# Kernel tuning notes

Measured on AMD Instinct MI355X. Metric: run time of the kernel, lower is better.

Reference implementation:

```python
import jax, jax.numpy as jnp
import numpy as np

NUM_STAGES = 3
EPS = 1e-6


def _l2norm(x, axis):
    return x / (EPS + jnp.linalg.norm(x, axis=axis, keepdims=True))


def _l1norm(x, axis):
    return x / (EPS + jnp.sum(x, axis=axis, keepdims=True))


def setup_inputs() -> dict:
    key = jax.random.key(0)
    k1, k2 = jax.random.split(key)
    B, C, H, W, K = 16, 512, 64, 64, 64
    feats = jax.random.normal(k1, (B, C, H, W), dtype=jnp.float32)
    # bases buffer: N(0, sqrt(2/K)) then l2-normalized along channel dim (done in reference)
    bases = jax.random.normal(k2, (1, C, K), dtype=jnp.float32) * np.sqrt(2.0 / K)
    return {"feats": feats, "bases": bases}


def reference(feats, bases):
    B, C, H, W = feats.shape
    f = feats.reshape(B, C, H * W)              # [B, C, N]
    b = _l2norm(bases, axis=1)                  # match buffer init normalization
    b = jnp.broadcast_to(b, (B, C, b.shape[2])) # [B, C, K]
    attention = None
    for _ in range(NUM_STAGES):
        attention = jnp.einsum('bcn,bck->bnk', f, b)        # [B, N, K]
        attention = jax.nn.softmax(attention, axis=2)
        attention_normed = _l1norm(attention, axis=1)
        b = jnp.einsum('bcn,bnk->bck', f, attention_normed)  # [B, C, K]
        b = _l2norm(b, axis=1)
    # EM loop runs under torch.no_grad in the original
    b = jax.lax.stop_gradient(b)
    attention = jax.lax.stop_gradient(attention)
    feats_recon = jnp.einsum('bck,bnk->bcn', b, attention)   # [B, C, N]
    return feats_recon.reshape(B, C, H, W)
```

## Files before the change

### kernel.cpp

```cpp
#include <hip/hip_runtime.h>
#include <stdint.h>

#define B_ 16
#define C_ 512
#define N_ 4096
#define K_ 64
#define NUM_STAGES 3

typedef __bf16 bf16x8 __attribute__((ext_vector_type(8)));
typedef float f32x4 __attribute__((ext_vector_type(4)));

__device__ __forceinline__ uint16_t f2bf(float x) {
  union { float f; uint32_t u; } v; v.f = x;
  uint32_t r = (v.u + 0x7FFFu + ((v.u >> 16) & 1u)) >> 16;
  return (uint16_t)r;
}

__device__ __forceinline__ void async16(const uint16_t* g, uint16_t* l) {
  __builtin_amdgcn_global_load_lds(
      (const __attribute__((address_space(1))) unsigned int*)g,
      (__attribute__((address_space(3))) unsigned int*)l, 16, 0, 0);
}

__global__ __launch_bounds__(256) void k_prep(const float* __restrict__ feats,
                                              uint16_t* __restrict__ f16,
                                              uint16_t* __restrict__ fT16) {
  __shared__ uint16_t tile[64][65];
  int b = blockIdx.z, c0 = blockIdx.y * 64, n0 = blockIdx.x * 64;
  int t = threadIdx.x;
  const float* src = feats + ((size_t)b * C_ + c0) * N_ + n0;
  uint16_t* dst = f16 + ((size_t)b * C_ + c0) * N_ + n0;
  int cl = t >> 4;
  int nl = (t & 15) * 4;
#pragma unroll
  for (int i = 0; i < 4; ++i) {
    int c = cl + 16 * i;
    float4 v = *(const float4*)(src + (size_t)c * N_ + nl);
    ushort4 x;
    x.x = f2bf(v.x); x.y = f2bf(v.y); x.z = f2bf(v.z); x.w = f2bf(v.w);
    *(ushort4*)(dst + (size_t)c * N_ + nl) = x;
    tile[c][nl + 0] = x.x; tile[c][nl + 1] = x.y;
    tile[c][nl + 2] = x.z; tile[c][nl + 3] = x.w;
  }
  __syncthreads();
  uint16_t* dstT = fT16 + ((size_t)b * N_ + n0) * C_ + c0;
#pragma unroll
  for (int i = 0; i < 4; ++i) {
    int n = cl + 16 * i;
    int c = nl;
    ushort4 y;
    y.x = tile[c + 0][n]; y.y = tile[c + 1][n];
    y.z = tile[c + 2][n]; y.w = tile[c + 3][n];
    *(ushort4*)(dstT + (size_t)n * C_ + c) = y;
  }
}

__global__ __launch_bounds__(256) void k_init_basis(const float* __restrict__ bases,
                                                    uint16_t* __restrict__ basis,
                                                    uint16_t* __restrict__ basisT) {
  int b = blockIdx.x;
  int t = threadIdx.x;
  __shared__ float red[256];
  __shared__ float inv[64];
  int k = t & 63;
  float s = 0.f;
  for (int c = (t >> 6); c < C_; c += 4) {
    float v = bases[c * K_ + k];
    s += v * v;
  }
  red[t] = s;
  __syncthreads();
  if (t < 64) {
    float tot = red[t] + red[t + 64] + red[t + 128] + red[t + 192];
    inv[t] = 1.f / (1e-6f + sqrtf(tot));
  }
  __syncthreads();
  uint16_t* ob = basis + (size_t)b * C_ * K_;
  for (int i = 0; i < (C_ * K_) / 256; ++i) {
    int idx = t + 256 * i;
    int kk = idx & 63;
    ob[idx] = f2bf(bases[idx] * inv[kk]);
  }
  uint16_t* obT = basisT + (size_t)b * K_ * C_;
  for (int i = 0; i < (C_ * K_) / 256; ++i) {
    int idx = t + 256 * i;
    int kk = idx >> 9;
    int cc = idx & 511;
    obT[idx] = f2bf(bases[cc * K_ + kk] * inv[kk]);
  }
}

__global__ __launch_bounds__(256) void k_gemm1(const uint16_t* __restrict__ fT,
                                               const uint16_t* __restrict__ basisT,
                                               uint16_t* __restrict__ attn,
                                               uint16_t* __restrict__ attnT,
                                               int write_attn) {
  __shared__ __attribute__((aligned(16))) uint16_t ldsA[64 * 64];
  __shared__ __attribute__((aligned(16))) uint16_t ldsB[64 * 64];
  int b = blockIdx.y;
  int n0 = blockIdx.x * 64;
  int t = threadIdx.x;
  int w = t >> 6, lane = t & 63, l15 = lane & 15, quad = lane >> 4;
  const uint16_t* A = fT + ((size_t)b * N_ + n0) * C_;
  const uint16_t* Bm = basisT + (size_t)b * K_ * C_;
  f32x4 acc[4] = {};
  for (int cs = 0; cs < C_; cs += 64) {
    __syncthreads();
#pragma unroll
    for (int r = 0; r < 2; ++r) {
      int e = r * 256 + t;
      int row = e >> 3, ch = e & 7;
      int sch = (ch + row) & 7;
      async16(A + (size_t)row * C_ + cs + sch * 8, ldsA + (r * 256 + (t & 192)) * 8);
    }
#pragma unroll
    for (int r = 0; r < 2; ++r) {
      int e = r * 256 + t;
      int row = e >> 3, ch = e & 7;
      int sch = (ch + row) & 7;
      async16(Bm + (size_t)row * C_ + cs + sch * 8, ldsB + (r * 256 + (t & 192)) * 8);
    }
    __syncthreads();
#pragma unroll
    for (int s = 0; s < 2; ++s) {
      int cc = s * 4 + quad;
      int ra = 16 * w + l15;
      bf16x8 af = *(const bf16x8*)(ldsA + (ra * 8 + ((cc - ra) & 7)) * 8);
#pragma unroll
      for (int t4 = 0; t4 < 4; ++t4) {
        int rb = 16 * t4 + l15;
        bf16x8 bv = *(const bf16x8*)(ldsB + (rb * 8 + ((cc - rb) & 7)) * 8);
        acc[t4] = __builtin_amdgcn_mfma_f32_16x16x32_bf16(af, bv, acc[t4], 0, 0, 0);
      }
    }
  }
  float p[4][4];
#pragma unroll
  for (int r = 0; r < 4; ++r) {
    float m = fmaxf(fmaxf(acc[0][r], acc[1][r]), fmaxf(acc[2][r], acc[3][r]));
    m = fmaxf(m, __shfl_xor(m, 1));
    m = fmaxf(m, __shfl_xor(m, 2));
    m = fmaxf(m, __shfl_xor(m, 4));
    m = fmaxf(m, __shfl_xor(m, 8));
    float s = 0.f;
#pragma unroll
    for (int t4 = 0; t4 < 4; ++t4) { p[t4][r] = __expf(acc[t4][r] - m); s += p[t4][r]; }
    s += __shfl_xor(s, 1); s += __shfl_xor(s, 2);
    s += __shfl_xor(s, 4); s += __shfl_xor(s, 8);
    float inv = 1.f / s;
#pragma unroll
    for (int t4 = 0; t4 < 4; ++t4) p[t4][r] *= inv;
  }
  if (write_attn) {
    uint16_t* oa = attn + ((size_t)b * N_ + n0 + 16 * w + quad * 4) * K_;
#pragma unroll
    for (int r = 0; r < 4; ++r) {
#pragma unroll
      for (int t4 = 0; t4 < 4; ++t4) oa[(size_t)r * K_ + 16 * t4 + l15] = f2bf(p[t4][r]);
    }
  }
#pragma unroll
  for (int t4 = 0; t4 < 4; ++t4) {
    ushort4 y;
    y.x = f2bf(p[t4][0]); y.y = f2bf(p[t4][1]);
    y.z = f2bf(p[t4][2]); y.w = f2bf(p[t4][3]);
    *(ushort4*)(attnT + ((size_t)b * K_ + 16 * t4 + l15) * N_ + n0 + 16 * w + quad * 4) = y;
  }
}

__global__ __launch_bounds__(256) void k_gemm2(const uint16_t* __restrict__ f16,
                                               const uint16_t* __restrict__ attnT,
                                               float* __restrict__ brawT) {
  __shared__ __attribute__((aligned(16))) uint16_t ldsA[32 * 64];
  __shared__ __attribute__((aligned(16))) uint16_t ldsB[64 * 64];
  int b = blockIdx.z;
  int c0 = blockIdx.x * 32;
  int slice = blockIdx.y;
  int ns0 = slice * 1024;
  int t = threadIdx.x, w = t >> 6, lane = t & 63, l15 = lane & 15, quad = lane >> 4;
  int h = w >> 1, kh = w & 1;
  const uint16_t* A = f16 + ((size_t)b * C_ + c0) * N_;
  const uint16_t* Bm = attnT + (size_t)b * K_ * N_;
  f32x4 acc[2] = {};
  for (int ns = ns0; ns < ns0 + 1024; ns += 64) {
    __syncthreads();
    {
      int row = t >> 3, ch = t & 7;
      int sch = (ch + row) & 7;
      async16(A + (size_t)row * N_ + ns + sch * 8, ldsA + (t & 192) * 8);
    }
#pragma unroll
    for (int r = 0; r < 2; ++r) {
      int e = r * 256 + t;
      int row = e >> 3, ch = e & 7;
      int sch = (ch + row) & 7;
      async16(Bm + (size_t)row * N_ + ns + sch * 8, ldsB + (r * 256 + (t & 192)) * 8);
    }
    __syncthreads();
#pragma unroll
    for (int s = 0; s < 2; ++s) {
      int cc = s * 4 + quad;
      int ra = 16 * h + l15;
      bf16x8 af = *(const bf16x8*)(ldsA + (ra * 8 + ((cc - ra) & 7)) * 8);
#pragma unroll
      for (int t2 = 0; t2 < 2; ++t2) {
        int rb = 32 * kh + 16 * t2 + l15;
        bf16x8 bv = *(const bf16x8*)(ldsB + (rb * 8 + ((cc - rb) & 7)) * 8);
        acc[t2] = __builtin_amdgcn_mfma_f32_16x16x32_bf16(af, bv, acc[t2], 0, 0, 0);
      }
    }
  }
  float* out = brawT + ((size_t)slice * B_ + b) * K_ * C_;
#pragma unroll
  for (int t2 = 0; t2 < 2; ++t2) {
    int k = 32 * kh + 16 * t2 + l15;
    float4 v = make_float4(acc[t2][0], acc[t2][1], acc[t2][2], acc[t2][3]);
    *(float4*)(out + (size_t)k * C_ + c0 + 16 * h + quad * 4) = v;
  }
}

__global__ __launch_bounds__(256) void k_l2fused(const float* __restrict__ brawT,
                                                 uint16_t* __restrict__ basisT,
                                                 uint16_t* __restrict__ basis) {
  __shared__ float red[4][128];
  __shared__ float invs[4];
  int b = blockIdx.x, kg = blockIdx.y;
  int t = threadIdx.x;
  int c4 = (t & 127) * 4;
  int khalf = t >> 7;
  float4 bs[2];
  float pr[2];
#pragma unroll
  for (int i = 0; i < 2; ++i) {
    int k = kg * 4 + khalf * 2 + i;
    float4 a = make_float4(0.f, 0.f, 0.f, 0.f);
#pragma unroll
    for (int s = 0; s < 4; ++s) {
      const float* rp = brawT + (((size_t)s * B_ + b) * K_ + k) * C_ + c4;
      float4 v = *(const float4*)rp;
      a.x += v.x; a.y += v.y; a.z += v.z; a.w += v.w;
    }
    bs[i] = a;
    pr[i] = a.x * a.x + a.y * a.y + a.z * a.z + a.w * a.w;
  }
  red[khalf * 2 + 0][t & 127] = pr[0];
  red[khalf * 2 + 1][t & 127] = pr[1];
  __syncthreads();
  if (t < 4) {
    float s = 0.f;
#pragma unroll
    for (int j = 0; j < 128; ++j) s += red[t][j];
    invs[t] = 1.f / (1e-6f + sqrtf(s));
  }
  __syncthreads();
#pragma unroll
  for (int i = 0; i < 2; ++i) {
    int kk = khalf * 2 + i;
    int k = kg * 4 + kk;
    float inv = invs[kk];
    ushort4 y;
    y.x = f2bf(bs[i].x * inv); y.y = f2bf(bs[i].y * inv);
    y.z = f2bf(bs[i].z * inv); y.w = f2bf(bs[i].w * inv);
    *(ushort4*)(basisT + ((size_t)b * K_ + k) * C_ + c4) = y;
    uint16_t* ob = basis + (size_t)b * C_ * K_ + k;
    ob[(size_t)(c4 + 0) * K_] = y.x;
    ob[(size_t)(c4 + 1) * K_] = y.y;
    ob[(size_t)(c4 + 2) * K_] = y.z;
    ob[(size_t)(c4 + 3) * K_] = y.w;
  }
}

__global__ __launch_bounds__(256) void k_recon(const uint16_t* __restrict__ attn,
                                               const uint16_t* __restrict__ basis,
                                               float* __restrict__ out) {
  __shared__ __attribute__((aligned(16))) char smem[64 * 68 * 4];
  uint16_t* ldsA = (uint16_t*)smem;
  uint16_t* ldsB = (uint16_t*)(smem + 8192);
  float* ldsT = (float*)smem;
  int b = blockIdx.z, c0 = blockIdx.y * 64, n0 = blockIdx.x * 64;
  int t = threadIdx.x, w = t >> 6, lane = t & 63, l15 = lane & 15, quad = lane >> 4;
  const uint16_t* A = attn + ((size_t)b * N_ + n0) * K_;
  const uint16_t* Bm = basis + ((size_t)b * C_ + c0) * K_;
#pragma unroll
  for (int r = 0; r < 2; ++r) {
    int e = r * 256 + t;
    int row = e >> 3, ch = e & 7, sch = (ch + row) & 7;
    async16(A + (size_t)row * K_ + sch * 8, ldsA + (r * 256 + (t & 192)) * 8);
  }
#pragma unroll
  for (int r = 0; r < 2; ++r) {
    int e = r * 256 + t;
    int row = e >> 3, ch = e & 7, sch = (ch + row) & 7;
    async16(Bm + (size_t)row * K_ + sch * 8, ldsB + (r * 256 + (t & 192)) * 8);
  }
  f32x4 acc[4] = {};
  __syncthreads();
#pragma unroll
  for (int s = 0; s < 2; ++s) {
    int cc = s * 4 + quad;
    int ra = 16 * w + l15;
    bf16x8 af = *(const bf16x8*)(ldsA + (ra * 8 + ((cc - ra) & 7)) * 8);
#pragma unroll
    for (int t4 = 0; t4 < 4; ++t4) {
      int rb = 16 * t4 + l15;
      bf16x8 bv = *(const bf16x8*)(ldsB + (rb * 8 + ((cc - rb) & 7)) * 8);
      acc[t4] = __builtin_amdgcn_mfma_f32_16x16x32_bf16(af, bv, acc[t4], 0, 0, 0);
    }
  }
  __syncthreads();
#pragma unroll
  for (int t4 = 0; t4 < 4; ++t4) {
    float4 v = make_float4(acc[t4][0], acc[t4][1], acc[t4][2], acc[t4][3]);
    *(float4*)(ldsT + (size_t)(16 * t4 + l15) * 68 + 16 * w + quad * 4) = v;
  }
  __syncthreads();
  float* op = out + ((size_t)b * C_ + c0) * N_ + n0;
#pragma unroll
  for (int j = 0; j < 16; ++j) {
    int c = 4 * j + w;
    op[(size_t)c * N_ + lane] = ldsT[(size_t)c * 68 + lane];
  }
}

extern "C" void kernel_launch(void* const* d_in, const int* in_sizes, int n_in,
                              void* d_out, int out_size, void* d_ws, size_t ws_size,
                              hipStream_t stream) {
  const float* feats = (const float*)d_in[0];
  const float* bases = (const float*)d_in[1];
  float* out = (float*)d_out;
  char* ws = (char*)d_ws;
  uint16_t* f16 = (uint16_t*)(ws);
  uint16_t* fT16 = (uint16_t*)(ws + 67108864);
  uint16_t* attn = (uint16_t*)(ws + 134217728);
  uint16_t* attnT = (uint16_t*)(ws + 142606336);
  uint16_t* basis = (uint16_t*)(ws + 150994944);
  uint16_t* basisT = (uint16_t*)(ws + 152043520);
  float* brawT = (float*)(ws + 153092096);

  k_prep<<<dim3(64, 8, 16), 256, 0, stream>>>(feats, f16, fT16);
  k_init_basis<<<16, 256, 0, stream>>>(bases, basis, basisT);
  for (int st = 0; st < NUM_STAGES; ++st) {
    k_gemm1<<<dim3(64, 16), 256, 0, stream>>>(fT16, basisT, attn, attnT,
                                              st == NUM_STAGES - 1 ? 1 : 0);
    k_gemm2<<<dim3(16, 4, 16), 256, 0, stream>>>(f16, attnT, brawT);
    k_l2fused<<<dim3(16, 16), 256, 0, stream>>>(brawT, basisT, basis);
  }
  k_recon<<<dim3(64, 8, 16), 256, 0, stream>>>(attn, basis, out);
}
```

Measured before the change: 447.6 us.

## Widen prep transpose tiles, vectorize recon stores, shuffle-reduce l2 norms

The prep kernel now handles 128x128 tiles with 16-byte loads and stores. It packs bf16 pairs into 32-bit words in an XOR-swizzled LDS tile, so the transposed write of fT16 uses full 16-byte stores instead of 8-byte ones. The recon epilogue writes float4 per thread instead of scalar floats. The l2 norm reduction replaces a serial 128-element loop on four threads with wave shuffles. These changes target memory-transaction efficiency and a serialized reduction, at the cost of fewer, larger prep blocks and more complex swizzle indexing.

```diff
diff --git a/kernel.cpp b/kernel.cpp
--- a/kernel.cpp
+++ b/kernel.cpp
@@ -25,33 +25,51 @@
 __global__ __launch_bounds__(256) void k_prep(const float* __restrict__ feats,
                                               uint16_t* __restrict__ f16,
                                               uint16_t* __restrict__ fT16) {
-  __shared__ uint16_t tile[64][65];
-  int b = blockIdx.z, c0 = blockIdx.y * 64, n0 = blockIdx.x * 64;
+  __shared__ uint32_t tile[128][64];
+  int b = blockIdx.z, c0 = blockIdx.y * 128, n0 = blockIdx.x * 128;
   int t = threadIdx.x;
+  int rl = t >> 4;
+  int g = t & 15;
   const float* src = feats + ((size_t)b * C_ + c0) * N_ + n0;
   uint16_t* dst = f16 + ((size_t)b * C_ + c0) * N_ + n0;
-  int cl = t >> 4;
-  int nl = (t & 15) * 4;
-#pragma unroll
-  for (int i = 0; i < 4; ++i) {
-    int c = cl + 16 * i;
-    float4 v = *(const float4*)(src + (size_t)c * N_ + nl);
-    ushort4 x;
-    x.x = f2bf(v.x); x.y = f2bf(v.y); x.z = f2bf(v.z); x.w = f2bf(v.w);
-    *(ushort4*)(dst + (size_t)c * N_ + nl) = x;
-    tile[c][nl + 0] = x.x; tile[c][nl + 1] = x.y;
-    tile[c][nl + 2] = x.z; tile[c][nl + 3] = x.w;
+#pragma unroll
+  for (int i = 0; i < 8; ++i) {
+    int c = rl + 16 * i;
+    int n8 = g * 8;
+    float4 v0 = *(const float4*)(src + (size_t)c * N_ + n8);
+    float4 v1 = *(const float4*)(src + (size_t)c * N_ + n8 + 4);
+    uint32_t q0 = (uint32_t)f2bf(v0.x) | ((uint32_t)f2bf(v0.y) << 16);
+    uint32_t q1 = (uint32_t)f2bf(v0.z) | ((uint32_t)f2bf(v0.w) << 16);
+    uint32_t q2 = (uint32_t)f2bf(v1.x) | ((uint32_t)f2bf(v1.y) << 16);
+    uint32_t q3 = (uint32_t)f2bf(v1.z) | ((uint32_t)f2bf(v1.w) << 16);
+    *(uint4*)(dst + (size_t)c * N_ + n8) = make_uint4(q0, q1, q2, q3);
+    int h = 2 * ((c >> 3) & 15);
+    int base = (4 * g) ^ (h & 28);
+    int p = h & 3;
+    uint32_t w[4];
+    w[0 ^ p] = q0; w[1 ^ p] = q1; w[2 ^ p] = q2; w[3 ^ p] = q3;
+    *(uint4*)&tile[c][base] = make_uint4(w[0], w[1], w[2], w[3]);
   }
   __syncthreads();
   uint16_t* dstT = fT16 + ((size_t)b * N_ + n0) * C_ + c0;
 #pragma unroll
-  for (int i = 0; i < 4; ++i) {
-    int n = cl + 16 * i;
-    int c = nl;
-    ushort4 y;
-    y.x = tile[c + 0][n]; y.y = tile[c + 1][n];
-    y.z = tile[c + 2][n]; y.w = tile[c + 3][n];
-    *(ushort4*)(dstT + (size_t)n * C_ + c) = y;
+  for (int i = 0; i < 8; ++i) {
+    int n = rl + 16 * i;
+    int s = n >> 1, half = (n & 1) * 16;
+    int c8 = g * 8;
+    uint16_t e[8];
+#pragma unroll
+    for (int j = 0; j < 8; ++j) {
+      int c = c8 + j;
+      int h = 2 * ((c >> 3) & 15);
+      uint32_t u = tile[c][s ^ h];
+      e[j] = (uint16_t)(u >> half);
+    }
+    uint32_t q0 = (uint32_t)e[0] | ((uint32_t)e[1] << 16);
+    uint32_t q1 = (uint32_t)e[2] | ((uint32_t)e[3] << 16);
+    uint32_t q2 = (uint32_t)e[4] | ((uint32_t)e[5] << 16);
+    uint32_t q3 = (uint32_t)e[6] | ((uint32_t)e[7] << 16);
+    *(uint4*)(dstT + (size_t)n * C_ + c8) = make_uint4(q0, q1, q2, q3);
   }
 }
 
@@ -225,7 +243,7 @@
   __shared__ float red[4][128];
   __shared__ float invs[4];
   int b = blockIdx.x, kg = blockIdx.y;
-  int t = threadIdx.x;
+  int t = threadIdx.x, lane = t & 63;
   int c4 = (t & 127) * 4;
   int khalf = t >> 7;
   float4 bs[2];
@@ -246,11 +264,12 @@
   red[khalf * 2 + 0][t & 127] = pr[0];
   red[khalf * 2 + 1][t & 127] = pr[1];
   __syncthreads();
-  if (t < 4) {
-    float s = 0.f;
-#pragma unroll
-    for (int j = 0; j < 128; ++j) s += red[t][j];
-    invs[t] = 1.f / (1e-6f + sqrtf(s));
+  {
+    int g = t >> 6;
+    float s = red[g][lane] + red[g][lane + 64];
+    s += __shfl_xor(s, 1); s += __shfl_xor(s, 2); s += __shfl_xor(s, 4);
+    s += __shfl_xor(s, 8); s += __shfl_xor(s, 16); s += __shfl_xor(s, 32);
+    if (lane == 0) invs[g] = 1.f / (1e-6f + sqrtf(s));
   }
   __syncthreads();
 #pragma unroll
@@ -315,10 +334,11 @@
   }
   __syncthreads();
   float* op = out + ((size_t)b * C_ + c0) * N_ + n0;
-#pragma unroll
-  for (int j = 0; j < 16; ++j) {
-    int c = 4 * j + w;
-    op[(size_t)c * N_ + lane] = ldsT[(size_t)c * 68 + lane];
+  int n4 = l15 * 4;
+#pragma unroll
+  for (int j = 0; j < 4; ++j) {
+    int c = 16 * j + 4 * w + quad;
+    *(float4*)(op + (size_t)c * N_ + n4) = *(const float4*)(ldsT + (size_t)c * 68 + n4);
   }
 }
 
@@ -337,7 +357,7 @@
   uint16_t* basisT = (uint16_t*)(ws + 152043520);
   float* brawT = (float*)(ws + 153092096);
 
-  k_prep<<<dim3(64, 8, 16), 256, 0, stream>>>(feats, f16, fT16);
+  k_prep<<<dim3(32, 4, 16), 256, 0, stream>>>(feats, f16, fT16);
   k_init_basis<<<16, 256, 0, stream>>>(bases, basis, basisT);
   for (int st = 0; st < NUM_STAGES; ++st) {
     k_gemm1<<<dim3(64, 16), 256, 0, stream>>>(fT16, basisT, attn, attnT,
```

Result: no change. 445.5 us (-0.5%).
